# Kernel optimization log

Hardware: AMD Instinct MI355X
Metric: run time of the kernel (lower is better)

## Reference

```python
import jax, jax.numpy as jnp
import numpy as np

EPS = 1e-5

def _layernorm(h):
    # parameter-free LayerNorm over last dim (elementwise_affine=False)
    mu = jnp.mean(h, axis=-1, keepdims=True)
    var = jnp.mean(jnp.square(h - mu), axis=-1, keepdims=True)
    return (h - mu) / jnp.sqrt(var + EPS)

def setup_inputs() -> dict:
    key = jax.random.key(0)
    k1, k2, k3, k4 = jax.random.split(key, 4)
    B, D, F_, I = 16, 37, 4096, 64
    x = jax.random.normal(k1, (B, D, F_), dtype=jnp.float32)
    s = 1.0 / np.sqrt(D)  # ~ torch Linear default init scale
    Wq = jax.random.normal(k2, (D, I), dtype=jnp.float32) * s
    Wk = jax.random.normal(k3, (D, I), dtype=jnp.float32) * s
    Wv = jax.random.normal(k4, (D, I), dtype=jnp.float32) * s
    return {"x": x, "Wq": Wq, "Wk": Wk, "Wv": Wv}

def reference(x, Wq, Wk, Wv):
    # x: [B, depth, featuresize] -> entities [B, F, depth]
    xb = jnp.transpose(x, (0, 2, 1))
    q = _layernorm(jnp.einsum('bfd,di->bfi', xb, Wq))
    k = _layernorm(jnp.einsum('bfd,di->bfi', xb, Wk))
    v = _layernorm(jnp.einsum('bfd,di->bfi', xb, Wv))
    d = q.shape[-1]
    att = jnp.einsum('bqi,bki->bqk', q, k) / jnp.sqrt(jnp.float32(d))
    # faithful to torch: softmax over dim=1 (the query axis), not the key axis
    weights = jax.nn.softmax(att, axis=-2)
    return jnp.einsum('bqk,bki->bqi', weights, v)
```

## Files before the change

### kernel.cpp

```cpp
#include <hip/hip_runtime.h>
#include <math.h>

#define B_  16
#define D_  37
#define F_  4096
#define I_  64
#define EPS 1e-5f
#define QSCALE 0.18033688011112042f
#define NQS 2
#define NKS 2

typedef unsigned short u16;
typedef __bf16 bf16x8 __attribute__((ext_vector_type(8)));
typedef __bf16 bf16x2v __attribute__((ext_vector_type(2)));
typedef float  f32x16 __attribute__((ext_vector_type(16)));
typedef float  f32x2v __attribute__((ext_vector_type(2)));
typedef unsigned int u32x4 __attribute__((ext_vector_type(4)));
typedef int i32x2 __attribute__((ext_vector_type(2)));

#define ZERO16 {0,0,0,0, 0,0,0,0, 0,0,0,0, 0,0,0,0}
#define MFMA32(a, b, c) __builtin_amdgcn_mfma_f32_32x32x16_bf16((a), (b), (c), 0, 0, 0)

#if __has_builtin(__builtin_amdgcn_exp2f)
#define EX2(x) __builtin_amdgcn_exp2f(x)
#else
#define EX2(x) exp2f(x)
#endif
#if __has_builtin(__builtin_amdgcn_rcpf)
#define RCP(x) __builtin_amdgcn_rcpf(x)
#else
#define RCP(x) (1.f / (x))
#endif

__device__ __forceinline__ u16 f2b(float f) {
  unsigned u = __builtin_bit_cast(unsigned, f);
  return (u16)((u + 0x7fffu + ((u >> 16) & 1u)) >> 16);
}
__device__ __forceinline__ float b2f(u16 h) {
  return __builtin_bit_cast(float, (unsigned)h << 16);
}
__device__ __forceinline__ unsigned pk2(float lo, float hi) {
  f32x2v f = {lo, hi};
  bf16x2v h = __builtin_convertvector(f, bf16x2v);
  return __builtin_bit_cast(unsigned, h);
}

__device__ __forceinline__ void plswap(unsigned& a, unsigned& b) {
#if __has_builtin(__builtin_amdgcn_permlane32_swap)
  i32x2 r = __builtin_amdgcn_permlane32_swap((int)a, (int)b, false, false);
  a = (unsigned)r[0];
  b = (unsigned)r[1];
#else
  const int lh = (int)((threadIdx.x & 63) >> 5);
  unsigned pa = (unsigned)__shfl_xor((int)a, 32, 64);
  unsigned pb = (unsigned)__shfl_xor((int)b, 32, 64);
  unsigned na = lh ? pb : a;
  unsigned nb = lh ? b : pa;
  a = na;
  b = nb;
#endif
}

__device__ __forceinline__ void build_af(const f32x16& s, bf16x8& f0, bf16x8& f1) {
  float e[16];
#pragma unroll
  for (int r = 0; r < 16; ++r) e[r] = EX2(s[r]);
  unsigned a = pk2(e[0], e[1]),   bq = pk2(e[2], e[3]);
  unsigned c = pk2(e[4], e[5]),   d  = pk2(e[6], e[7]);
  plswap(a, c);
  plswap(bq, d);
  u32x4 v0 = {a, bq, c, d};
  f0 = __builtin_bit_cast(bf16x8, v0);
  unsigned ee = pk2(e[8], e[9]),  ff = pk2(e[10], e[11]);
  unsigned g  = pk2(e[12], e[13]), h = pk2(e[14], e[15]);
  plswap(ee, g);
  plswap(ff, h);
  u32x4 v1 = {ee, ff, g, h};
  f1 = __builtin_bit_cast(bf16x8, v1);
}

__device__ __forceinline__ bf16x8 ldfrag(const u16* base, int row, int kb) {
  return *(const bf16x8*)(base + (row << 6) + ((kb ^ (row & 7)) << 3));
}
__device__ __forceinline__ int soff_l(int c) {
  const int r = c >> 3, cb = c & 7;
  return (r << 6) + ((cb ^ (r & 7)) << 3);
}
__device__ __forceinline__ int soff_g(int c, int spitch) {
  return (c >> 3) * spitch + ((c & 7) << 3);
}

__device__ __forceinline__ int swz512(int wg) {
  return (wg & 7) * 64 + (wg >> 3);
}

__global__ __launch_bounds__(256) void qkv_ln_k(
    const float* __restrict__ x,
    const float* __restrict__ Wq, const float* __restrict__ Wk,
    const float* __restrict__ Wv,
    u16* __restrict__ qn, u16* __restrict__ kn, u16* __restrict__ vt) {
  __shared__ __align__(16) float xs[64 * 44];
  __shared__ __align__(16) u16 vtile[64 * 72];

  const int t = threadIdx.x;
  const int b = blockIdx.y;
  const int f0 = blockIdx.x * 64;
  const int lane = t & 63, w = t >> 6;

  float wq[40], wk[40], wv[40];
#pragma unroll
  for (int d = 0; d < D_; ++d) {
    wq[d] = Wq[d * I_ + lane];
    wk[d] = Wk[d * I_ + lane];
    wv[d] = Wv[d * I_ + lane];
  }
#pragma unroll
  for (int d = D_; d < 40; ++d) { wq[d] = 0.f; wk[d] = 0.f; wv[d] = 0.f; }

  const float* xb = x + (size_t)b * D_ * F_ + f0;
  for (int i = t; i < D_ * 64; i += 256) {
    const int d = i >> 6, fl = i & 63;
    xs[fl * 44 + d] = xb[(size_t)d * F_ + fl];
  }
  if (t < 192) {
    const int fl = t / 3, dp = 37 + (t % 3);
    xs[fl * 44 + dp] = 0.f;
  }
  __syncthreads();

  for (int it = 0; it < 16; ++it) {
    const int fl = w * 16 + it;
    const float* xr = &xs[fl * 44];
    float hq = 0.f, hk = 0.f, hv = 0.f;
#pragma unroll
    for (int j = 0; j < 10; ++j) {
      const float4 xv = *(const float4*)(xr + j * 4);
      hq = fmaf(xv.x, wq[4*j+0], hq); hk = fmaf(xv.x, wk[4*j+0], hk); hv = fmaf(xv.x, wv[4*j+0], hv);
      hq = fmaf(xv.y, wq[4*j+1], hq); hk = fmaf(xv.y, wk[4*j+1], hk); hv = fmaf(xv.y, wv[4*j+1], hv);
      hq = fmaf(xv.z, wq[4*j+2], hq); hk = fmaf(xv.z, wk[4*j+2], hk); hv = fmaf(xv.z, wv[4*j+2], hv);
      hq = fmaf(xv.w, wq[4*j+3], hq); hk = fmaf(xv.w, wk[4*j+3], hk); hv = fmaf(xv.w, wv[4*j+3], hv);
    }
    auto lnorm = [&](float a) -> float {
      float s = a;
#pragma unroll
      for (int o = 32; o > 0; o >>= 1) s += __shfl_xor(s, o, 64);
      const float mu = s * (1.f / 64.f);
      const float d0 = a - mu;
      float v = d0 * d0;
#pragma unroll
      for (int o = 32; o > 0; o >>= 1) v += __shfl_xor(v, o, 64);
      return d0 * rsqrtf(v * (1.f / 64.f) + EPS);
    };
    const size_t fo = ((size_t)b * F_ + f0 + fl) * I_ + lane;
    qn[fo] = f2b(lnorm(hq) * QSCALE);
    kn[fo] = f2b(lnorm(hk));
    vtile[lane * 72 + fl] = f2b(lnorm(hv));
  }
  __syncthreads();
  for (int p = 0; p < 2; ++p) {
    const int c = p * 256 + t;
    const int r = c >> 3, off = (c & 7) * 8;
    const int4 v = *(const int4*)&vtile[r * 72 + off];
    *(int4*)(vt + ((size_t)b * I_ + r) * F_ + f0 + off) = v;
  }
}

__global__ __launch_bounds__(256, 2) void attn_stats_k(
    const u16* __restrict__ qn, const u16* __restrict__ kn,
    float* __restrict__ zp) {
  __shared__ __align__(16) u16 sm[16384];

  const int t = threadIdx.x, lane = t & 63, w = t >> 6;
  const int l31 = lane & 31, lh = lane >> 5;
  const int lg = swz512((int)blockIdx.x);
  const int k0 = (lg & 15) * 256, b = (lg >> 4) & 15, qh = lg >> 8;

  const u16* kp = kn + ((size_t)b * F_ + k0 + w * 64 + l31) * I_ + lh * 8;
  bf16x8 kf[2][4];
#pragma unroll
  for (int kb2 = 0; kb2 < 2; ++kb2)
#pragma unroll
    for (int ic = 0; ic < 4; ++ic)
      kf[kb2][ic] = *(const bf16x8*)(kp + kb2 * 32 * I_ + ic * 16);

  int qoff_l[2], qoff_g[2];
#pragma unroll
  for (int p = 0; p < 2; ++p) {
    const int c = p * 256 + t;
    qoff_l[p] = soff_l(c);
    qoff_g[p] = soff_g(c, 64);
  }

  const u16* qsrc = qn + ((size_t)b * F_ + qh * (F_ / NQS)) * I_;
#pragma unroll
  for (int s = 0; s < 2; ++s)
#pragma unroll
    for (int p = 0; p < 2; ++p)
      *(int4*)(sm + s * 4096 + qoff_l[p]) =
          *(const int4*)(qsrc + s * 64 * I_ + qoff_g[p]);
  qsrc += 128 * I_;

  float Zc[2][2] = {{0.f, 0.f}, {0.f, 0.f}};

  auto Mg = [&](const u16* Qc, int qb, f32x16& t0, f32x16& t1) {
    __builtin_amdgcn_s_setprio(1);
#pragma unroll
    for (int ic = 0; ic < 4; ++ic) {
      const bf16x8 qv = ldfrag(Qc + qb * 32 * 64, l31, ic * 2 + lh);
      t0 = MFMA32(qv, kf[0][ic], t0);
      t1 = MFMA32(qv, kf[1][ic], t1);
    }
    __builtin_amdgcn_s_setprio(0);
  };
  auto Eg = [&](int qb, const f32x16& t0, const f32x16& t1) {
#pragma unroll
    for (int r = 0; r < 16; ++r) {
      Zc[qb][0] += EX2(t0[r]);
      Zc[qb][1] += EX2(t1[r]);
    }
  };

  const int NC = F_ / NQS / 128;

  for (int c = 0; c < NC; ++c) {
    const int cur = (c & 1) * 8192;
    const int nxt = cur ^ 8192;
    const bool pf = (c + 1 < NC);
    __syncthreads();
    int4 qr0, qr1;
    if (pf) {
      qr0 = *(const int4*)(qsrc + qoff_g[0]);
      qr1 = *(const int4*)(qsrc + qoff_g[1]);
    }

    f32x16 sA0 = ZERO16, sA1 = ZERO16;
    Mg(sm + cur, 0, sA0, sA1);
    f32x16 sB0 = ZERO16, sB1 = ZERO16;
    Mg(sm + cur, 1, sB0, sB1);
    Eg(0, sA0, sA1);

    if (pf) {
      *(int4*)(sm + nxt + qoff_l[0]) = qr0;
      *(int4*)(sm + nxt + qoff_l[1]) = qr1;
      qr0 = *(const int4*)(qsrc + 64 * I_ + qoff_g[0]);
      qr1 = *(const int4*)(qsrc + 64 * I_ + qoff_g[1]);
    }

    f32x16 sC0 = ZERO16, sC1 = ZERO16;
    Mg(sm + cur + 4096, 0, sC0, sC1);
    Eg(1, sB0, sB1);
    f32x16 sD0 = ZERO16, sD1 = ZERO16;
    Mg(sm + cur + 4096, 1, sD0, sD1);
    Eg(0, sC0, sC1);

    if (pf) {
      *(int4*)(sm + nxt + 4096 + qoff_l[0]) = qr0;
      *(int4*)(sm + nxt + 4096 + qoff_l[1]) = qr1;
      qsrc += 128 * I_;
    }
    Eg(1, sD0, sD1);
  }

#pragma unroll
  for (int kb2 = 0; kb2 < 2; ++kb2) {
    float Zt = Zc[0][kb2] + Zc[1][kb2];
    Zt += __shfl_xor(Zt, 32, 64);
    if (lane < 32)
      zp[((size_t)qh * B_ + b) * F_ + k0 + w * 64 + kb2 * 32 + lane] = Zt;
  }
}

__global__ __launch_bounds__(256, 2) void attn_out_k(
    const u16* __restrict__ qn, const u16* __restrict__ kn,
    const u16* __restrict__ vt, const float* __restrict__ zp,
    float* __restrict__ out, u16* __restrict__ pout) {
  __shared__ __align__(16) u16 sm[32768];
  __shared__ __align__(16) float rzs[F_ / NKS];

  const int t = threadIdx.x, lane = t & 63, w = t >> 6;
  const int l31 = lane & 31, lh = lane >> 5;
  const int lg = swz512((int)blockIdx.x);
  const int q0 = (lg & 15) * 256, b = (lg >> 4) & 15, ks = lg >> 8;

  {
    const float* z0p = zp + (size_t)b * F_ + ks * (F_ / NKS);
    const float* z1p = z0p + (size_t)B_ * F_;
    const int k8 = t * 8;
    const float4 a0 = *(const float4*)(z0p + k8);
    const float4 a1 = *(const float4*)(z0p + k8 + 4);
    const float4 b0 = *(const float4*)(z1p + k8);
    const float4 b1 = *(const float4*)(z1p + k8 + 4);
    float4 r0, r1;
    r0.x = RCP(a0.x + b0.x); r0.y = RCP(a0.y + b0.y);
    r0.z = RCP(a0.z + b0.z); r0.w = RCP(a0.w + b0.w);
    r1.x = RCP(a1.x + b1.x); r1.y = RCP(a1.y + b1.y);
    r1.z = RCP(a1.z + b1.z); r1.w = RCP(a1.w + b1.w);
    *(float4*)(rzs + k8)     = r0;
    *(float4*)(rzs + k8 + 4) = r1;
  }
  __syncthreads();

  const u16* qp = qn + ((size_t)b * F_ + q0 + w * 64 + l31) * I_ + lh * 8;
  bf16x8 qf[2][4];
#pragma unroll
  for (int qb2 = 0; qb2 < 2; ++qb2)
#pragma unroll
    for (int ic = 0; ic < 4; ++ic)
      qf[qb2][ic] = *(const bf16x8*)(qp + qb2 * 32 * I_ + ic * 16);

  int off_l[2], kg[2], vg[2];
#pragma unroll
  for (int p = 0; p < 2; ++p) {
    const int c = p * 256 + t;
    off_l[p] = soff_l(c);
    kg[p] = soff_g(c, 64);
    vg[p] = soff_g(c, F_);
  }
  const int kw = (t & 7) * 8;

  auto vscale16 = [&](int4 raw, int kb) -> int4 {
    u16 es[8];
    *(int4*)es = raw;
    const float4 r0 = *(const float4*)(rzs + kb);
    const float4 r1 = *(const float4*)(rzs + kb + 4);
    unsigned o01 = pk2(b2f(es[0]) * r0.x, b2f(es[1]) * r0.y);
    unsigned o23 = pk2(b2f(es[2]) * r0.z, b2f(es[3]) * r0.w);
    unsigned o45 = pk2(b2f(es[4]) * r1.x, b2f(es[5]) * r1.y);
    unsigned o67 = pk2(b2f(es[6]) * r1.z, b2f(es[7]) * r1.w);
    u32x4 o = {o01, o23, o45, o67};
    return __builtin_bit_cast(int4, o);
  };

  const u16* ksrc = kn + ((size_t)b * F_ + ks * (F_ / NKS)) * I_;
  const u16* vsrc = vt + (size_t)b * I_ * F_ + ks * (F_ / NKS);
#pragma unroll
  for (int s = 0; s < 2; ++s)
#pragma unroll
    for (int p = 0; p < 2; ++p) {
      *(int4*)(sm + s * 4096 + off_l[p]) =
          *(const int4*)(ksrc + s * 64 * I_ + kg[p]);
      *(int4*)(sm + 16384 + s * 4096 + off_l[p]) =
          vscale16(*(const int4*)(vsrc + s * 64 + vg[p]), s * 64 + kw);
    }
  ksrc += 128 * I_;
  vsrc += 128;

  f32x16 o00 = ZERO16, o01 = ZERO16, o10 = ZERO16, o11 = ZERO16;

  auto Sg = [&](const u16* Kc, f32x16& t0, f32x16& t1) {
    __builtin_amdgcn_s_setprio(1);
#pragma unroll
    for (int ic = 0; ic < 4; ++ic) {
      const bf16x8 ak = ldfrag(Kc, l31, ic * 2 + lh);
      t0 = MFMA32(ak, qf[0][ic], t0);
      t1 = MFMA32(ak, qf[1][ic], t1);
    }
    __builtin_amdgcn_s_setprio(0);
  };
  auto EPg = [&](const u16* Vc, int kh, const f32x16& t0, const f32x16& t1) {
    bf16x8 a0, a1, b0, b1;
    build_af(t0, a0, a1);
    build_af(t1, b0, b1);
    __builtin_amdgcn_s_setprio(1);
    {
      const int kb4 = kh * 2;
      const bf16x8 bv0 = ldfrag(Vc, l31, kb4 * 2 + lh);
      const bf16x8 bv1 = ldfrag(Vc + 32 * 64, l31, kb4 * 2 + lh);
      o00 = MFMA32(a0, bv0, o00);
      o01 = MFMA32(a0, bv1, o01);
      o10 = MFMA32(b0, bv0, o10);
      o11 = MFMA32(b0, bv1, o11);
    }
    {
      const int kb4 = kh * 2 + 1;
      const bf16x8 bv0 = ldfrag(Vc, l31, kb4 * 2 + lh);
      const bf16x8 bv1 = ldfrag(Vc + 32 * 64, l31, kb4 * 2 + lh);
      o00 = MFMA32(a1, bv0, o00);
      o01 = MFMA32(a1, bv1, o01);
      o10 = MFMA32(b1, bv0, o10);
      o11 = MFMA32(b1, bv1, o11);
    }
    __builtin_amdgcn_s_setprio(0);
  };

  const int NC = F_ / NKS / 128;

  for (int c = 0; c < NC; ++c) {
    const int cur = (c & 1) * 8192;
    const int nxt = cur ^ 8192;
    const bool pf = (c + 1 < NC);
    const int kc = (c + 1) * 128;
    __syncthreads();
    int4 kr0, kr1, vr0, vr1;
    if (pf) {
      kr0 = *(const int4*)(ksrc + kg[0]);
      kr1 = *(const int4*)(ksrc + kg[1]);
      vr0 = *(const int4*)(vsrc + vg[0]);
      vr1 = *(const int4*)(vsrc + vg[1]);
    }

    const u16* K0 = sm + cur;
    const u16* V0 = sm + 16384 + cur;
    const u16* K1 = K0 + 4096;
    const u16* V1 = V0 + 4096;

    f32x16 sA0 = ZERO16, sA1 = ZERO16;
    Sg(K0, sA0, sA1);
    f32x16 sB0 = ZERO16, sB1 = ZERO16;
    Sg(K0 + 32 * 64, sB0, sB1);
    EPg(V0, 0, sA0, sA1);

    if (pf) {
      *(int4*)(sm + nxt + off_l[0])         = kr0;
      *(int4*)(sm + nxt + off_l[1])         = kr1;
      *(int4*)(sm + 16384 + nxt + off_l[0]) = vscale16(vr0, kc + kw);
      *(int4*)(sm + 16384 + nxt + off_l[1]) = vscale16(vr1, kc + kw);
      kr0 = *(const int4*)(ksrc + 64 * I_ + kg[0]);
      kr1 = *(const int4*)(ksrc + 64 * I_ + kg[1]);
      vr0 = *(const int4*)(vsrc + 64 + vg[0]);
      vr1 = *(const int4*)(vsrc + 64 + vg[1]);
    }

    f32x16 sC0 = ZERO16, sC1 = ZERO16;
    Sg(K1, sC0, sC1);
    EPg(V0, 1, sB0, sB1);
    f32x16 sD0 = ZERO16, sD1 = ZERO16;
    Sg(K1 + 32 * 64, sD0, sD1);
    EPg(V1, 0, sC0, sC1);

    if (pf) {
      *(int4*)(sm + nxt + 4096 + off_l[0])         = kr0;
      *(int4*)(sm + nxt + 4096 + off_l[1])         = kr1;
      *(int4*)(sm + 16384 + nxt + 4096 + off_l[0]) = vscale16(vr0, kc + 64 + kw);
      *(int4*)(sm + 16384 + nxt + 4096 + off_l[1]) = vscale16(vr1, kc + 64 + kw);
      ksrc += 128 * I_;
      vsrc += 128;
    }
    EPg(V1, 1, sD0, sD1);
  }

  if (ks == 0) {
    float* ob = out + ((size_t)b * F_ + q0 + w * 64) * I_;
#pragma unroll
    for (int r = 0; r < 16; ++r) {
      const int qr = (r & 3) + 8 * (r >> 2) + 4 * lh;
      ob[(size_t)qr * I_ + l31]              = o00[r];
      ob[(size_t)qr * I_ + 32 + l31]         = o01[r];
      ob[(size_t)(32 + qr) * I_ + l31]       = o10[r];
      ob[(size_t)(32 + qr) * I_ + 32 + l31]  = o11[r];
    }
  } else {
    u16* pb = pout + ((size_t)b * F_ + q0 + w * 64) * I_;
#pragma unroll
    for (int r = 0; r < 16; ++r) {
      const int qr = (r & 3) + 8 * (r >> 2) + 4 * lh;
      pb[(size_t)qr * I_ + l31]              = f2b(o00[r]);
      pb[(size_t)qr * I_ + 32 + l31]         = f2b(o01[r]);
      pb[(size_t)(32 + qr) * I_ + l31]       = f2b(o10[r]);
      pb[(size_t)(32 + qr) * I_ + 32 + l31]  = f2b(o11[r]);
    }
  }
}

__global__ __launch_bounds__(256) void reduce_k(float* __restrict__ out,
                                                const u16* __restrict__ pout) {
  const size_t i = ((size_t)blockIdx.x * 256 + threadIdx.x) * 8;
  float4 a0 = *(const float4*)(out + i);
  float4 a1 = *(const float4*)(out + i + 4);
  int4 praw = *(const int4*)(pout + i);
  u16 es[8];
  *(int4*)es = praw;
  a0.x += b2f(es[0]); a0.y += b2f(es[1]); a0.z += b2f(es[2]); a0.w += b2f(es[3]);
  a1.x += b2f(es[4]); a1.y += b2f(es[5]); a1.z += b2f(es[6]); a1.w += b2f(es[7]);
  *(float4*)(out + i)     = a0;
  *(float4*)(out + i + 4) = a1;
}

extern "C" void kernel_launch(void* const* d_in, const int* in_sizes, int n_in,
                              void* d_out, int out_size, void* d_ws,
                              size_t ws_size, hipStream_t stream) {
  const float* x  = (const float*)d_in[0];
  const float* Wq = (const float*)d_in[1];
  const float* Wk = (const float*)d_in[2];
  const float* Wv = (const float*)d_in[3];
  float* out = (float*)d_out;

  const size_t NBF = (size_t)B_ * F_ * I_;
  u16* qn   = (u16*)d_ws;
  u16* kn   = qn + NBF;
  u16* vt   = kn + NBF;
  float* zp = (float*)(vt + NBF);
  u16* pout = (u16*)(zp + (size_t)NQS * B_ * F_);

  qkv_ln_k<<<dim3(F_ / 64, B_), 256, 0, stream>>>(x, Wq, Wk, Wv, qn, kn, vt);
  attn_stats_k<<<dim3(512), 256, 0, stream>>>(qn, kn, zp);
  attn_out_k<<<dim3(512), 256, 0, stream>>>(qn, kn, vt, zp, out, pout);
  reduce_k<<<dim3((int)(NBF / 2048)), 256, 0, stream>>>(out, pout);
}
```

Before: 226.0 us.

## Widen key tile per wave in stats kernel to reuse query fragments

The softmax-denominator kernel now gives each wave 128 keys instead of 64 and splits the query axis into four parts instead of two. Each query fragment read from LDS then feeds four key blocks instead of two, which halves LDS fragment reads per MFMA and halves query streaming per block. The output kernel is updated to sum four partial denominators before taking the reciprocal. In exchange, the key fragments held in registers double, which may raise register pressure. The partial-sum buffer also grows and must be sized for four partials.

```diff
diff --git a/kernel.cpp b/kernel.cpp
--- a/kernel.cpp
+++ b/kernel.cpp
@@ -7,7 +7,7 @@
 #define I_  64
 #define EPS 1e-5f
 #define QSCALE 0.18033688011112042f
-#define NQS 2
+#define NQS 4
 #define NKS 2
 
 typedef unsigned short u16;
@@ -173,12 +173,12 @@
   const int t = threadIdx.x, lane = t & 63, w = t >> 6;
   const int l31 = lane & 31, lh = lane >> 5;
   const int lg = swz512((int)blockIdx.x);
-  const int k0 = (lg & 15) * 256, b = (lg >> 4) & 15, qh = lg >> 8;
-
-  const u16* kp = kn + ((size_t)b * F_ + k0 + w * 64 + l31) * I_ + lh * 8;
-  bf16x8 kf[2][4];
-#pragma unroll
-  for (int kb2 = 0; kb2 < 2; ++kb2)
+  const int k0 = (lg & 7) * 512, b = (lg >> 3) & 15, qh = lg >> 7;
+
+  const u16* kp = kn + ((size_t)b * F_ + k0 + w * 128 + l31) * I_ + lh * 8;
+  bf16x8 kf[4][4];
+#pragma unroll
+  for (int kb2 = 0; kb2 < 4; ++kb2)
 #pragma unroll
     for (int ic = 0; ic < 4; ++ic)
       kf[kb2][ic] = *(const bf16x8*)(kp + kb2 * 32 * I_ + ic * 16);
@@ -200,23 +200,27 @@
           *(const int4*)(qsrc + s * 64 * I_ + qoff_g[p]);
   qsrc += 128 * I_;
 
-  float Zc[2][2] = {{0.f, 0.f}, {0.f, 0.f}};
-
-  auto Mg = [&](const u16* Qc, int qb, f32x16& t0, f32x16& t1) {
+  float Zc[2][4] = {{0.f,0.f,0.f,0.f},{0.f,0.f,0.f,0.f}};
+
+  auto LQ = [&](const u16* Qc, int qb, bf16x8 qv[4]) {
+#pragma unroll
+    for (int ic = 0; ic < 4; ++ic)
+      qv[ic] = ldfrag(Qc + qb * 32 * 64, l31, ic * 2 + lh);
+  };
+  auto Mg = [&](const bf16x8 qv[4], int kbp, f32x16& t0, f32x16& t1) {
     __builtin_amdgcn_s_setprio(1);
 #pragma unroll
     for (int ic = 0; ic < 4; ++ic) {
-      const bf16x8 qv = ldfrag(Qc + qb * 32 * 64, l31, ic * 2 + lh);
-      t0 = MFMA32(qv, kf[0][ic], t0);
-      t1 = MFMA32(qv, kf[1][ic], t1);
+      t0 = MFMA32(qv[ic], kf[2 * kbp][ic], t0);
+      t1 = MFMA32(qv[ic], kf[2 * kbp + 1][ic], t1);
     }
     __builtin_amdgcn_s_setprio(0);
   };
-  auto Eg = [&](int qb, const f32x16& t0, const f32x16& t1) {
+  auto Eg = [&](int qb, int kbp, const f32x16& t0, const f32x16& t1) {
 #pragma unroll
     for (int r = 0; r < 16; ++r) {
-      Zc[qb][0] += EX2(t0[r]);
-      Zc[qb][1] += EX2(t1[r]);
+      Zc[qb][2 * kbp]     += EX2(t0[r]);
+      Zc[qb][2 * kbp + 1] += EX2(t1[r]);
     }
   };
 
@@ -233,11 +237,21 @@
       qr1 = *(const int4*)(qsrc + qoff_g[1]);
     }
 
-    f32x16 sA0 = ZERO16, sA1 = ZERO16;
-    Mg(sm + cur, 0, sA0, sA1);
-    f32x16 sB0 = ZERO16, sB1 = ZERO16;
-    Mg(sm + cur, 1, sB0, sB1);
-    Eg(0, sA0, sA1);
+    bf16x8 qvA[4];
+    LQ(sm + cur, 0, qvA);
+    f32x16 s00 = ZERO16, s01 = ZERO16;
+    Mg(qvA, 0, s00, s01);
+    f32x16 s02 = ZERO16, s03 = ZERO16;
+    Mg(qvA, 1, s02, s03);
+    Eg(0, 0, s00, s01);
+    bf16x8 qvB[4];
+    LQ(sm + cur, 1, qvB);
+    f32x16 s10 = ZERO16, s11 = ZERO16;
+    Mg(qvB, 0, s10, s11);
+    Eg(0, 1, s02, s03);
+    f32x16 s12 = ZERO16, s13 = ZERO16;
+    Mg(qvB, 1, s12, s13);
+    Eg(1, 0, s10, s11);
 
     if (pf) {
       *(int4*)(sm + nxt + qoff_l[0]) = qr0;
@@ -246,27 +260,37 @@
       qr1 = *(const int4*)(qsrc + 64 * I_ + qoff_g[1]);
     }
 
-    f32x16 sC0 = ZERO16, sC1 = ZERO16;
-    Mg(sm + cur + 4096, 0, sC0, sC1);
-    Eg(1, sB0, sB1);
-    f32x16 sD0 = ZERO16, sD1 = ZERO16;
-    Mg(sm + cur + 4096, 1, sD0, sD1);
-    Eg(0, sC0, sC1);
+    bf16x8 qvC[4];
+    LQ(sm + cur + 4096, 0, qvC);
+    f32x16 s20 = ZERO16, s21 = ZERO16;
+    Mg(qvC, 0, s20, s21);
+    Eg(1, 1, s12, s13);
+    f32x16 s22 = ZERO16, s23 = ZERO16;
+    Mg(qvC, 1, s22, s23);
+    Eg(0, 0, s20, s21);
+    bf16x8 qvD[4];
+    LQ(sm + cur + 4096, 1, qvD);
+    f32x16 s30 = ZERO16, s31 = ZERO16;
+    Mg(qvD, 0, s30, s31);
+    Eg(0, 1, s22, s23);
+    f32x16 s32 = ZERO16, s33 = ZERO16;
+    Mg(qvD, 1, s32, s33);
+    Eg(1, 0, s30, s31);
 
     if (pf) {
       *(int4*)(sm + nxt + 4096 + qoff_l[0]) = qr0;
       *(int4*)(sm + nxt + 4096 + qoff_l[1]) = qr1;
       qsrc += 128 * I_;
     }
-    Eg(1, sD0, sD1);
-  }
-
-#pragma unroll
-  for (int kb2 = 0; kb2 < 2; ++kb2) {
+    Eg(1, 1, s32, s33);
+  }
+
+#pragma unroll
+  for (int kb2 = 0; kb2 < 4; ++kb2) {
     float Zt = Zc[0][kb2] + Zc[1][kb2];
     Zt += __shfl_xor(Zt, 32, 64);
     if (lane < 32)
-      zp[((size_t)qh * B_ + b) * F_ + k0 + w * 64 + kb2 * 32 + lane] = Zt;
+      zp[((size_t)qh * B_ + b) * F_ + k0 + w * 128 + kb2 * 32 + lane] = Zt;
   }
 }
 
@@ -283,18 +307,21 @@
   const int q0 = (lg & 15) * 256, b = (lg >> 4) & 15, ks = lg >> 8;
 
   {
-    const float* z0p = zp + (size_t)b * F_ + ks * (F_ / NKS);
-    const float* z1p = z0p + (size_t)B_ * F_;
+    const float* zb = zp + (size_t)b * F_ + ks * (F_ / NKS);
+    const size_t PL = (size_t)B_ * F_;
     const int k8 = t * 8;
-    const float4 a0 = *(const float4*)(z0p + k8);
-    const float4 a1 = *(const float4*)(z0p + k8 + 4);
-    const float4 b0 = *(const float4*)(z1p + k8);
-    const float4 b1 = *(const float4*)(z1p + k8 + 4);
+    float4 s0 = *(const float4*)(zb + k8);
+    float4 s1 = *(const float4*)(zb + k8 + 4);
+#pragma unroll
+    for (int qh = 1; qh < NQS; ++qh) {
+      const float4 a0 = *(const float4*)(zb + qh * PL + k8);
+      const float4 a1 = *(const float4*)(zb + qh * PL + k8 + 4);
+      s0.x += a0.x; s0.y += a0.y; s0.z += a0.z; s0.w += a0.w;
+      s1.x += a1.x; s1.y += a1.y; s1.z += a1.z; s1.w += a1.w;
+    }
     float4 r0, r1;
-    r0.x = RCP(a0.x + b0.x); r0.y = RCP(a0.y + b0.y);
-    r0.z = RCP(a0.z + b0.z); r0.w = RCP(a0.w + b0.w);
-    r1.x = RCP(a1.x + b1.x); r1.y = RCP(a1.y + b1.y);
-    r1.z = RCP(a1.z + b1.z); r1.w = RCP(a1.w + b1.w);
+    r0.x = RCP(s0.x); r0.y = RCP(s0.y); r0.z = RCP(s0.z); r0.w = RCP(s0.w);
+    r1.x = RCP(s1.x); r1.y = RCP(s1.y); r1.z = RCP(s1.z); r1.w = RCP(s1.w);
     *(float4*)(rzs + k8)     = r0;
     *(float4*)(rzs + k8 + 4) = r1;
   }
```

Result: no change. 227.6 us (+0.7%).
